# Performance work log

Hardware: AMD Instinct MI355X
Metric: run time of the kernel (lower is better)

Reference implementation:

```python
import jax, jax.numpy as jnp
import numpy as np

B, H, N, D = 64, 12, 196, 768  # ViT-B/16 @ 224: 196 patch tokens + 1 CLS


def setup_inputs() -> dict:
    key = jax.random.key(0)
    k1, k2, k3 = jax.random.split(key, 3)
    student_tokens = jax.random.normal(k1, (B, N, D), dtype=jnp.float32)
    teacher_tokens = jax.random.normal(k2, (B, N, D), dtype=jnp.float32)
    teacher_attn = jax.random.uniform(k3, (B, H, N + 1, N + 1), dtype=jnp.float32)
    return {
        "student_tokens": student_tokens,
        "teacher_tokens": teacher_tokens,
        "teacher_attn": teacher_attn,
    }


def reference(student_tokens, teacher_tokens, teacher_attn):
    s = student_tokens.astype(jnp.float32)
    t = teacher_tokens.astype(jnp.float32)
    # CLS->patch attention, averaged over heads: [B, N]
    w = teacher_attn[:, :, 0, 1:].mean(axis=1)
    w = w / (w.sum(axis=-1, keepdims=True) + 1e-8)
    s = w[..., None] * s
    t = w[..., None] * t
    # center over token dim
    s_c = s - s.mean(axis=1, keepdims=True)
    t_c = t - t.mean(axis=1, keepdims=True)
    tr_s = jnp.sum(s_c * s_c, axis=(1, 2))  # [B]
    tr_t = jnp.sum(t_c * t_c, axis=(1, 2))  # [B]
    # cross-covariance: [B, D, D]
    cross = jnp.einsum("bnd,bne->bde", s_c, t_c)
    # nuclear norm = sum of singular values
    nuclear = jnp.linalg.svd(cross, compute_uv=False).sum(axis=-1)  # [B]
    loss = jnp.maximum(tr_s + tr_t - 2.0 * nuclear, 0.0).mean()
    return loss
```

## Files before the change

### kernel.cpp

```cpp
#include <hip/hip_runtime.h>
#include <hip/hip_bf16.h>
#include <math.h>

#define NTOK 196
#define NDIM 768
#define NB 64
#define NH 12
#define NA 197
#define MAT (NTOK * NTOK)
#define ATTN_HW (NA * NA)
#define POLAR_ITERS 15

#define PADC 208
#define NTILE 13
#define POLAR_LDS_BYTES (2 * NTOK * PADC * 2)

#define GCH 64
#define GPLANE (208 * GCH)
#define GRAM_LDS_BYTES (2 * GPLANE * 2)

#define POW_LD 197
#define POW_F_WORDS (NTOK * POW_LD)
#define POW_LDS_BYTES ((POW_F_WORDS + 2 * NTOK + 256) * 4)

#define PTLD 208
#define TRI_WORDS 19306
#define CHOL2_PT_WORDS (16 * PTLD)
#define CHOL2_TRI_OFF CHOL2_PT_WORDS
#define CHOL2_ROWOFF_OFF (CHOL2_TRI_OFF + TRI_WORDS)
#define CHOL2_PV_OFF 22832
#define CHOL2_LDS_BYTES ((CHOL2_PV_OFF + 32) * 4)

typedef __attribute__((ext_vector_type(8))) short short8;
typedef __attribute__((ext_vector_type(4))) short short4_t;
typedef __attribute__((ext_vector_type(4))) float f32x4;

__device__ inline short8 s8zero() { short8 z = {0,0,0,0,0,0,0,0}; return z; }

__device__ inline short f2bf(float f) {
  union { float f; unsigned u; } v; v.f = f;
  unsigned u = v.u;
  u += 0x7fffu + ((u >> 16) & 1u);
  return (short)(u >> 16);
}
__device__ inline float bf2f(short s) {
  union { unsigned u; float f; } v;
  v.u = ((unsigned)(unsigned short)s) << 16;
  return v.f;
}

__device__ inline int swz_g(int g, int r) {
  if (g < 16) return g ^ (r & 7);
  else if (g < 24) return 16 + ((g - 16) ^ (r & 7));
  else return 24 + ((g - 24) ^ (r & 1));
}

__global__ void k_w(const float* __restrict__ attn, float* __restrict__ wbuf) {
  int b = blockIdx.x;
  int tid = threadIdx.x;
  __shared__ float red[256];
  float w0 = 0.f;
  if (tid < NTOK) {
    size_t base = (size_t)b * NH * ATTN_HW + 1 + tid;
    #pragma unroll
    for (int h = 0; h < NH; ++h) w0 += attn[base + (size_t)h * ATTN_HW];
    w0 *= (1.f / NH);
  }
  red[tid] = (tid < NTOK) ? w0 : 0.f;
  __syncthreads();
  for (int s = 128; s > 0; s >>= 1) { if (tid < s) red[tid] += red[tid + s]; __syncthreads(); }
  float S = red[0];
  if (tid < NTOK) wbuf[b * NTOK + tid] = w0 / (S + 1e-8f);
}

__global__ __launch_bounds__(512, 1) void k_gram_mfma(
    const float* __restrict__ s, const float* __restrict__ t,
    const float* __restrict__ wbuf, float* __restrict__ Gbuf) {
  extern __shared__ short gsm[];
  short* bhp = gsm;
  short* blp = gsm + GPLANE;
  __shared__ float wsh[NTOK];
  int slot = blockIdx.x, b = slot >> 1, src = slot & 1;
  const float* X = (src ? t : s) + (size_t)b * NTOK * NDIM;
  int tid = threadIdx.x;
  int wave = tid >> 6, ln15 = tid & 15, quad = (tid >> 4) & 3;

  if (tid < NTOK) wsh[tid] = wbuf[b * NTOK + tid];
  for (int i = tid; i < 768; i += 512) {
    int p = i / 384, o = i - p * 384;
    ((int*)(gsm + p * GPLANE + 196 * GCH))[o] = 0;
  }
  __syncthreads();

  f32x4 zz = {0.f, 0.f, 0.f, 0.f};
  f32x4 acc[12];
  #pragma unroll
  for (int j = 0; j < 12; ++j) acc[j] = zz;

  for (int c = 0; c < NDIM / GCH; ++c) {
    int kc = c * GCH;
    for (int gi = tid; gi < NTOK * 8; gi += 512) {
      int r = gi >> 3, g = gi & 7;
      const float* sp = X + (size_t)r * NDIM + kc + g * 8;
      float4 f0 = *(const float4*)(sp);
      float4 f1 = *(const float4*)(sp + 4);
      float wv = wsh[r];
      float vs[8] = {f0.x, f0.y, f0.z, f0.w, f1.x, f1.y, f1.z, f1.w};
      short8 hv, lv;
      #pragma unroll
      for (int e = 0; e < 8; ++e) {
        float y = wv * vs[e];
        short hb = f2bf(y);
        hv[e] = hb;
        lv[e] = f2bf(y - bf2f(hb));
      }
      int pg = (g ^ (r & 7)) * 8;
      *(short8*)(bhp + r * GCH + pg) = hv;
      *(short8*)(blp + r * GCH + pg) = lv;
    }
    __syncthreads();
    #pragma unroll
    for (int j = 0; j < 12; ++j) {
      int T = wave + 8 * j;
      if (T < 91) {
        int ti = (int)((sqrtf(8.f * T + 1.f) - 1.f) * 0.5f);
        if ((ti + 1) * (ti + 2) / 2 <= T) ++ti;
        if (ti * (ti + 1) / 2 > T) --ti;
        int tj = T - ti * (ti + 1) / 2;
        int ra = ti * 16 + ln15, rb = tj * 16 + ln15;
        #pragma unroll
        for (int ks = 0; ks < 2; ++ks) {
          int gb0 = ks * 4 + quad;
          int ga = (gb0 ^ (ra & 7)) * 8, gb = (gb0 ^ (rb & 7)) * 8;
          short8 ah = *(const short8*)(bhp + ra * GCH + ga);
          short8 al = *(const short8*)(blp + ra * GCH + ga);
          short8 bhf = *(const short8*)(bhp + rb * GCH + gb);
          short8 blf = *(const short8*)(blp + rb * GCH + gb);
          acc[j] = __builtin_amdgcn_mfma_f32_16x16x32_bf16(ah, bhf, acc[j], 0, 0, 0);
          acc[j] = __builtin_amdgcn_mfma_f32_16x16x32_bf16(ah, blf, acc[j], 0, 0, 0);
          acc[j] = __builtin_amdgcn_mfma_f32_16x16x32_bf16(al, bhf, acc[j], 0, 0, 0);
        }
      }
    }
    __syncthreads();
  }

  float* G = Gbuf + (size_t)slot * MAT;
  #pragma unroll
  for (int j = 0; j < 12; ++j) {
    int T = wave + 8 * j;
    if (T < 91) {
      int ti = (int)((sqrtf(8.f * T + 1.f) - 1.f) * 0.5f);
      if ((ti + 1) * (ti + 2) / 2 <= T) ++ti;
      if (ti * (ti + 1) / 2 > T) --ti;
      int tj = T - ti * (ti + 1) / 2;
      int col = tj * 16 + ln15;
      #pragma unroll
      for (int r = 0; r < 4; ++r) {
        int row = ti * 16 + quad * 4 + r;
        if (row < NTOK && col < NTOK) {
          G[row * NTOK + col] = acc[j][r];
          if (ti != tj) G[col * NTOK + row] = acc[j][r];
        }
      }
    }
  }
}

__global__ void k_center(float* __restrict__ Gbuf, float* __restrict__ trPb) {
  int slot = blockIdx.x;
  float* A = Gbuf + (size_t)slot * MAT;
  __shared__ float r[NTOK];
  __shared__ float red[256];
  __shared__ float gsh, dsh;
  int tid = threadIdx.x;
  float acc = 0.f;
  if (tid < NTOK) {
    for (int m = 0; m < NTOK; ++m) acc += A[m * NTOK + tid];
    r[tid] = acc * (1.f / NTOK);
  }
  red[tid] = (tid < NTOK) ? acc * (1.f / NTOK) : 0.f;
  __syncthreads();
  for (int s = 128; s > 0; s >>= 1) { if (tid < s) red[tid] += red[tid + s]; __syncthreads(); }
  float g = red[0] * (1.f / NTOK);
  float tv = (tid < NTOK) ? (A[tid * NTOK + tid] - 2.f * r[tid] + g) : 0.f;
  __syncthreads();
  red[tid] = tv;
  __syncthreads();
  for (int s = 128; s > 0; s >>= 1) { if (tid < s) red[tid] += red[tid + s]; __syncthreads(); }
  if (tid == 0) {
    float tr = red[0];
    trPb[slot] = tr;
    gsh = g;
    dsh = 1e-4f * fmaxf(tr, 0.f) * (1.f / NTOK);
  }
  __syncthreads();
  float gg = gsh, dd = dsh;
  for (int idx = tid; idx < MAT; idx += 256) {
    int n = idx / NTOK, m = idx - n * NTOK;
    float v = A[idx] - r[n] - r[m] + gg;
    if (n == m) v += dd;
    A[idx] = v;
  }
}

__global__ __launch_bounds__(256, 1) void k_chol_panel(float* __restrict__ Gbuf) {
  extern __shared__ float smf[];
  float* Pt = smf;
  float* tri = smf + CHOL2_TRI_OFF;
  int* rowoff = (int*)(smf + CHOL2_ROWOFF_OFF);
  float* pvb = smf + CHOL2_PV_OFF;
  int slot = blockIdx.x;
  float* A = Gbuf + (size_t)slot * MAT;
  int tid = threadIdx.x;
  if (tid < NTOK) rowoff[tid] = tid * (tid + 1) / 2;
  __syncthreads();
  for (int idx = tid; idx < MAT; idx += 256) {
    int i = idx / NTOK, j = idx - i * NTOK;
    if (j <= i) tri[rowoff[i] + j] = A[idx];
  }
  __syncthreads();

  for (int k0 = 0; k0 < NTOK; k0 += 16) {
    int nb = (NTOK - k0 < 16) ? (NTOK - k0) : 16;
    int t = tid;
    int i = k0 + t;
    bool hasrow = (t < NTOK - k0);
    int ro = hasrow ? rowoff[i] : 0;

    float a[16];
    #pragma unroll
    for (int jj = 0; jj < 16; ++jj) a[jj] = 0.f;
    if (hasrow) {
      #pragma unroll
      for (int jj = 0; jj < 16; ++jj)
        if (jj < nb && k0 + jj <= i) a[jj] = tri[ro + k0 + jj];
    }

    #pragma unroll
    for (int jj = 0; jj < 16; ++jj) {
      bool cv = (jj < nb);
      if (cv && hasrow && t >= jj && t < nb) pvb[((jj & 1) << 4) + t] = a[jj];
      __syncthreads();
      if (cv && hasrow && t >= jj) {
        const float* pv = pvb + ((jj & 1) << 4);
        f32x4 p0 = *(const f32x4*)(pv);
        f32x4 p1 = *(const f32x4*)(pv + 4);
        f32x4 p2 = *(const f32x4*)(pv + 8);
        f32x4 p3 = *(const f32x4*)(pv + 12);
        float pvj = (jj < 4) ? p0[jj & 3] : (jj < 8) ? p1[jj & 3]
                   : (jj < 12) ? p2[jj & 3] : p3[jj & 3];
        float sq = sqrtf(fmaxf(pvj, 1e-20f));
        float pivinv = 1.f / sq;
        float v = a[jj] * pivinv;
        a[jj] = v;
        #pragma unroll
        for (int m = 0; m < 16; ++m) {
          if (m > jj) {
            float pvm = (m < 4) ? p0[m & 3] : (m < 8) ? p1[m & 3]
                       : (m < 12) ? p2[m & 3] : p3[m & 3];
            if (m < nb) a[m] -= v * (pvm * pivinv);
          }
        }
      }
    }

    if (hasrow) {
      #pragma unroll
      for (int jj = 0; jj < 16; ++jj)
        if (jj < nb && k0 + jj <= i) tri[ro + k0 + jj] = a[jj];
      if (t >= nb) {
        #pragma unroll
        for (int jj = 0; jj < 16; ++jj)
          if (jj < nb) Pt[jj * PTLD + i] = a[jj];
      }
    }
    __syncthreads();

    int k1 = k0 + nb;
    int nrem = NTOK - k1;
    if (nrem > 0) {
      int ntile = (nrem + 3) >> 2;
      int Ttot = ntile * (ntile + 1) / 2;
      for (int T = tid; T < Ttot; T += 256) {
        float disc = (2.f * ntile + 1.f) * (2.f * ntile + 1.f) - 8.f * (float)T;
        int tm = (int)((2.f * ntile + 1.f - sqrtf(fmaxf(disc, 0.f))) * 0.5f);
        if (tm > ntile - 1) tm = ntile - 1;
        if (tm < 0) tm = 0;
        #define FCOL(c) ((c) * ntile - (((c) * ((c) - 1)) >> 1))
        while (tm + 1 <= ntile - 1 && FCOL(tm + 1) <= T) ++tm;
        while (tm > 0 && FCOL(tm) > T) --tm;
        int ti = tm + (T - FCOL(tm));
        #undef FCOL
        int i0 = k1 + ti * 4, m0 = k1 + tm * 4;
        f32x4 acc0 = {0.f, 0.f, 0.f, 0.f};
        f32x4 acc1 = acc0, acc2 = acc0, acc3 = acc0;
        #pragma unroll
        for (int jj = 0; jj < 16; ++jj) {
          if (jj < nb) {
            f32x4 li = *(const f32x4*)(Pt + jj * PTLD + i0);
            f32x4 lm = *(const f32x4*)(Pt + jj * PTLD + m0);
            acc0 += lm * li[0];
            acc1 += lm * li[1];
            acc2 += lm * li[2];
            acc3 += lm * li[3];
          }
        }
        #define STORE_ROW(r, av)                                        \
          { int ii = i0 + (r);                                          \
            if (ii < NTOK) {                                            \
              int roi = rowoff[ii];                                     \
              if (m0 + 0 <= ii) tri[roi + m0 + 0] -= (av)[0];           \
              if (m0 + 1 <= ii) tri[roi + m0 + 1] -= (av)[1];           \
              if (m0 + 2 <= ii) tri[roi + m0 + 2] -= (av)[2];           \
              if (m0 + 3 <= ii) tri[roi + m0 + 3] -= (av)[3];           \
            } }
        STORE_ROW(0, acc0)
        STORE_ROW(1, acc1)
        STORE_ROW(2, acc2)
        STORE_ROW(3, acc3)
        #undef STORE_ROW
      }
    }
    __syncthreads();
  }

  for (int idx = tid; idx < MAT; idx += 256) {
    int i = idx / NTOK, j = idx - i * NTOK;
    A[idx] = (j <= i) ? tri[rowoff[i] + j] : 0.f;
  }
}

__global__ void k_chol_global(float* __restrict__ Gbuf) {
  int slot = blockIdx.x;
  float* A = Gbuf + (size_t)slot * MAT;
  __shared__ float col[NTOK];
  __shared__ float piv;
  int tid = threadIdx.x;
  for (int k = 0; k < NTOK; ++k) {
    if (tid == 0) { float p = sqrtf(fmaxf(A[k * NTOK + k], 1e-20f)); A[k * NTOK + k] = p; piv = p; }
    __syncthreads();
    float inv = 1.f / piv;
    for (int i = k + 1 + tid; i < NTOK; i += 256) {
      float v = A[i * NTOK + k] * inv;
      A[i * NTOK + k] = v;
      col[i] = v;
    }
    for (int j = k + 1 + tid; j < NTOK; j += 256) A[k * NTOK + j] = 0.f;
    __syncthreads();
    int nrem = NTOK - 1 - k;
    int total = nrem * (nrem + 1) / 2;
    for (int tt = tid; tt < total; tt += 256) {
      int a = (int)((sqrtf(8.f * tt + 1.f) - 1.f) * 0.5f);
      while ((a + 1) * (a + 2) / 2 <= tt) ++a;
      while (a * (a + 1) / 2 > tt) --a;
      int bb = tt - a * (a + 1) / 2;
      int i = k + 1 + a, j = k + 1 + bb;
      A[i * NTOK + j] -= col[i] * col[j];
    }
    __syncthreads();
  }
}

__global__ void k_F(const float* __restrict__ Gbuf, float* __restrict__ Fbuf) {
  int b = blockIdx.y;
  const float* Lp = Gbuf + (size_t)(2 * b) * MAT;
  const float* Lq = Gbuf + (size_t)(2 * b + 1) * MAT;
  int ti = blockIdx.x / 7, tj = blockIdx.x % 7;
  int ri = ti * 32, cj = tj * 32;
  __shared__ float As[32][33], Bs[32][33];
  int tid = threadIdx.x, ty = tid >> 4, tx = tid & 15;
  float a00 = 0, a01 = 0, a10 = 0, a11 = 0;
  for (int k0 = 0; k0 < NTOK; k0 += 32) {
    for (int l = tid; l < 1024; l += 256) {
      int kk = l >> 5, ii = l & 31;
      int krow = k0 + kk;
      As[kk][ii] = (krow < NTOK && ri + ii < NTOK) ? Lp[(size_t)krow * NTOK + ri + ii] : 0.f;
      Bs[kk][ii] = (krow < NTOK && cj + ii < NTOK) ? Lq[(size_t)krow * NTOK + cj + ii] : 0.f;
    }
    __syncthreads();
    #pragma unroll
    for (int kk = 0; kk < 32; ++kk) {
      float p0 = As[kk][ty], p1 = As[kk][ty + 16];
      float q0 = Bs[kk][tx], q1 = Bs[kk][tx + 16];
      a00 += p0 * q0; a01 += p0 * q1; a10 += p1 * q0; a11 += p1 * q1;
    }
    __syncthreads();
  }
  float* F = Fbuf + (size_t)b * MAT;
  int i0 = ri + ty, i1 = ri + ty + 16, j0 = cj + tx, j1 = cj + tx + 16;
  if (i0 < NTOK && j0 < NTOK) F[i0 * NTOK + j0] = a00;
  if (i0 < NTOK && j1 < NTOK) F[i0 * NTOK + j1] = a01;
  if (i1 < NTOK && j0 < NTOK) F[i1 * NTOK + j0] = a10;
  if (i1 < NTOK && j1 < NTOK) F[i1 * NTOK + j1] = a11;
}

__global__ __launch_bounds__(256, 1) void k_pow_lds(const float* __restrict__ Fbuf,
                                                    float* __restrict__ nrmb) {
  extern __shared__ float psm[];
  float* Fsh = psm;
  float* v = psm + POW_F_WORDS;
  float* u = v + NTOK;
  float* red = u + NTOK;
  int b = blockIdx.x;
  const float* F = Fbuf + (size_t)b * MAT;
  int tid = threadIdx.x;
  for (int idx = tid; idx < MAT; idx += 256) {
    int i = idx / NTOK, j = idx - i * NTOK;
    Fsh[i * POW_LD + j] = F[idx];
  }
  if (tid < NTOK) v[tid] = 1.f;
  __syncthreads();
  float lastsum = 1.f;
  for (int it = 0; it < 6; ++it) {
    if (tid < NTOK) {
      float a = 0.f;
      for (int j = 0; j < NTOK; ++j) a += Fsh[tid * POW_LD + j] * v[j];
      u[tid] = a;
    }
    __syncthreads();
    float a2 = 0.f;
    if (tid < NTOK) { for (int i = 0; i < NTOK; ++i) a2 += Fsh[i * POW_LD + tid] * u[i]; }
    red[tid] = (tid < NTOK) ? a2 * a2 : 0.f;
    __syncthreads();
    for (int s2 = 128; s2 > 0; s2 >>= 1) { if (tid < s2) red[tid] += red[tid + s2]; __syncthreads(); }
    float sum = red[0];
    lastsum = sum;
    float invn = rsqrtf(sum + 1e-30f);
    __syncthreads();
    if (tid < NTOK) v[tid] = a2 * invn;
    __syncthreads();
  }
  if (tid == 0) {
    float sig = sqrtf(sqrtf(lastsum));
    nrmb[b] = 1.f / (1.1f * sig + 1e-30f);
  }
}

__global__ void k_pow(const float* __restrict__ Fbuf, float* __restrict__ nrmb) {
  int b = blockIdx.x;
  const float* F = Fbuf + (size_t)b * MAT;
  __shared__ float v[NTOK], u[NTOK];
  __shared__ float red[256];
  int tid = threadIdx.x;
  if (tid < NTOK) v[tid] = 1.f;
  __syncthreads();
  float lastsum = 1.f;
  for (int it = 0; it < 6; ++it) {
    float a = 0.f;
    if (tid < NTOK) { for (int j = 0; j < NTOK; ++j) a += F[tid * NTOK + j] * v[j]; }
    __syncthreads();
    if (tid < NTOK) u[tid] = a;
    __syncthreads();
    float a2 = 0.f;
    if (tid < NTOK) { for (int i = 0; i < NTOK; ++i) a2 += F[i * NTOK + tid] * u[i]; }
    red[tid] = (tid < NTOK) ? a2 * a2 : 0.f;
    __syncthreads();
    for (int s = 128; s > 0; s >>= 1) { if (tid < s) red[tid] += red[tid + s]; __syncthreads(); }
    float sum = red[0];
    lastsum = sum;
    float invn = rsqrtf(sum + 1e-30f);
    __syncthreads();
    if (tid < NTOK) v[tid] = a2 * invn;
    __syncthreads();
  }
  if (tid == 0) {
    float sig = sqrtf(sqrtf(lastsum));
    nrmb[b] = 1.f / (1.1f * sig + 1e-30f);
  }
}

__global__ void k_scale(const float* __restrict__ Fbuf, const float* __restrict__ nrmb,
                        float* __restrict__ X) {
  int b = blockIdx.y;
  int idx = blockIdx.x * 256 + threadIdx.x;
  if (idx < MAT) X[(size_t)b * MAT + idx] = Fbuf[(size_t)b * MAT + idx] * nrmb[b];
}

__global__ __launch_bounds__(512, 1) void k_polar_fused(
    const float* __restrict__ Fbuf, const float* __restrict__ nrmb,
    float* __restrict__ Xout) {
  extern __shared__ short sm[];
  short* bufA = sm;
  short* bufB = sm + NTOK * PADC;
  int b = blockIdx.x;
  const float* F = Fbuf + (size_t)b * MAT;
  float* XO = Xout + (size_t)b * MAT;
  int tid = threadIdx.x;
  int wave = tid >> 6, ln15 = tid & 15, quad = (tid >> 4) & 3;
  int rt0 = wave, rt1 = wave + 8;
  bool has2 = (rt1 < NTILE);

  for (int i = tid; i < (2 * NTOK * PADC) / 2; i += 512) ((int*)sm)[i] = 0;
  __syncthreads();
  float invc = nrmb[b];
  for (int idx = tid; idx < MAT; idx += 512) {
    int i = idx / NTOK, j = idx - i * NTOK;
    bufA[i * PADC + swz_g(j >> 3, i) * 8 + (j & 7)] = f2bf(F[idx] * invc);
  }
  __syncthreads();

  int arow0 = rt0 * 16 + ln15;
  int arow1 = rt1 * 16 + ln15;
  bool av1 = has2 && (arow1 < NTOK);
  int m0a = rt0 * 16 + quad * 4;
  int m1a = rt1 * 16 + quad * 4;
  int gq0 = 2 * rt0 + (quad >> 1);
  int gq1 = 2 * rt1 + (quad >> 1);
  int wsub = (quad & 1) * 4;
  int ga0 = arow0 >> 3, go0 = arow0 & 7;
  int ga1 = arow1 >> 3, go1 = arow1 & 7;

  for (int it = 0; it < POLAR_ITERS; ++it) {
    {
      short8 a0[7], a1[7];
      #pragma unroll
      for (int ks = 0; ks < 7; ++ks) {
        int kk = ks * 32 + quad * 8;
        int g = ks * 4 + quad;
        a0[ks] = (kk < PADC) ? *(const short8*)(bufA + arow0 * PADC + swz_g(g, arow0) * 8)
                             : s8zero();
        a1[ks] = (av1 && kk < PADC)
                     ? *(const short8*)(bufA + arow1 * PADC + swz_g(g, arow1) * 8)
                     : s8zero();
      }
      for (int ct = 0; ct < NTILE; ++ct) {
        int brow = ct * 16 + ln15;
        bool bv = brow < NTOK;
        f32x4 acc0 = {0.f, 0.f, 0.f, 0.f};
        f32x4 acc1 = {0.f, 0.f, 0.f, 0.f};
        #pragma unroll
        for (int ks = 0; ks < 7; ++ks) {
          int kk = ks * 32 + quad * 8;
          int g = ks * 4 + quad;
          short8 bfr = (bv && kk < PADC)
                           ? *(const short8*)(bufA + brow * PADC + swz_g(g, brow) * 8)
                           : s8zero();
          acc0 = __builtin_amdgcn_mfma_f32_16x16x32_bf16(a0[ks], bfr, acc0, 0, 0, 0);
          if (has2)
            acc1 = __builtin_amdgcn_mfma_f32_16x16x32_bf16(a1[ks], bfr, acc1, 0, 0, 0);
        }
        if (bv) {
          short4_t w0;
          #pragma unroll
          for (int r = 0; r < 4; ++r) {
            float h = -0.5f * acc0[r] + ((m0a + r == brow) ? 1.5f : 0.f);
            w0[r] = f2bf(h);
          }
          *(short4_t*)(bufB + brow * PADC + swz_g(gq0, brow) * 8 + wsub) = w0;
          if (has2) {
            short4_t w1;
            #pragma unroll
            for (int r = 0; r < 4; ++r) {
              float h = -0.5f * acc1[r] + ((m1a + r == brow) ? 1.5f : 0.f);
              w1[r] = f2bf(h);
            }
            *(short4_t*)(bufB + brow * PADC + swz_g(gq1, brow) * 8 + wsub) = w1;
          }
        }
      }
    }
    __syncthreads();
    {
      short8 g0[7], g1[7];
      #pragma unroll
      for (int ks = 0; ks < 7; ++ks) {
        int kk = ks * 32 + quad * 8;
        short8 v0 = s8zero(), v1 = s8zero();
        if (kk < PADC) {
          #pragma unroll
          for (int j = 0; j < 8; ++j) {
            int rr = kk + j;
            v0[j] = bufA[rr * PADC + swz_g(ga0, rr) * 8 + go0];
            if (has2) v1[j] = bufA[rr * PADC + swz_g(ga1, rr) * 8 + go1];
          }
        }
        g0[ks] = v0; g1[ks] = v1;
      }
      __syncthreads();
      for (int ct = 0; ct < NTILE; ++ct) {
        int n = ct * 16 + ln15;
        bool nv = n < NTOK;
        f32x4 acc0 = {0.f, 0.f, 0.f, 0.f};
        f32x4 acc1 = {0.f, 0.f, 0.f, 0.f};
        #pragma unroll
        for (int ks = 0; ks < 7; ++ks) {
          int kk = ks * 32 + quad * 8;
          int g = ks * 4 + quad;
          short8 bfr = (nv && kk < PADC)
                           ? *(const short8*)(bufB + n * PADC + swz_g(g, n) * 8)
                           : s8zero();
          acc0 = __builtin_amdgcn_mfma_f32_16x16x32_bf16(g0[ks], bfr, acc0, 0, 0, 0);
          if (has2)
            acc1 = __builtin_amdgcn_mfma_f32_16x16x32_bf16(g1[ks], bfr, acc1, 0, 0, 0);
        }
        if (nv) {
          short4_t w0;
          #pragma unroll
          for (int r = 0; r < 4; ++r) w0[r] = f2bf(acc0[r]);
          *(short4_t*)(bufA + n * PADC + swz_g(gq0, n) * 8 + wsub) = w0;
          if (has2) {
            short4_t w1;
            #pragma unroll
            for (int r = 0; r < 4; ++r) w1[r] = f2bf(acc1[r]);
            *(short4_t*)(bufA + n * PADC + swz_g(gq1, n) * 8 + wsub) = w1;
          }
        }
      }
    }
    __syncthreads();
  }

  for (int idx = tid; idx < MAT; idx += 512) {
    int i = idx / NTOK, j = idx - i * NTOK;
    XO[idx] = bf2f(bufA[i * PADC + swz_g(j >> 3, i) * 8 + (j & 7)]);
  }
}

__global__ void k_xtx(const float* __restrict__ Xb, float* __restrict__ Gp) {
  int b = blockIdx.y;
  const float* X = Xb + (size_t)b * MAT;
  int x = blockIdx.x, ti = 0;
  while (x >= ti + 1) { x -= ti + 1; ++ti; }
  int tj = x;
  int ri = ti * 32, cj = tj * 32;
  __shared__ float As[32][33], Bs[32][33];
  int tid = threadIdx.x, ty = tid >> 4, tx = tid & 15;
  float a00 = 0, a01 = 0, a10 = 0, a11 = 0;
  for (int k0 = 0; k0 < NTOK; k0 += 32) {
    for (int l = tid; l < 1024; l += 256) {
      int kk = l >> 5, ii = l & 31;
      int krow = k0 + kk;
      As[kk][ii] = (krow < NTOK && ri + ii < NTOK) ? X[(size_t)krow * NTOK + ri + ii] : 0.f;
      Bs[kk][ii] = (krow < NTOK && cj + ii < NTOK) ? X[(size_t)krow * NTOK + cj + ii] : 0.f;
    }
    __syncthreads();
    #pragma unroll
    for (int kk = 0; kk < 32; ++kk) {
      float p0 = As[kk][ty], p1 = As[kk][ty + 16];
      float q0 = Bs[kk][tx], q1 = Bs[kk][tx + 16];
      a00 += p0 * q0; a01 += p0 * q1; a10 += p1 * q0; a11 += p1 * q1;
    }
    __syncthreads();
  }
  float* G = Gp + (size_t)b * MAT;
  int i0 = ri + ty, i1 = ri + ty + 16, j0 = cj + tx, j1 = cj + tx + 16;
  if (i0 < NTOK && j0 < NTOK) { G[i0 * NTOK + j0] = a00; G[j0 * NTOK + i0] = a00; }
  if (i0 < NTOK && j1 < NTOK) { G[i0 * NTOK + j1] = a01; G[j1 * NTOK + i0] = a01; }
  if (i1 < NTOK && j0 < NTOK) { G[i1 * NTOK + j0] = a10; G[j0 * NTOK + i1] = a10; }
  if (i1 < NTOK && j1 < NTOK) { G[i1 * NTOK + j1] = a11; G[j1 * NTOK + i1] = a11; }
}

__global__ void k_nsup(const float* __restrict__ Xb, const float* __restrict__ Gp,
                       float* __restrict__ Xn) {
  int b = blockIdx.y;
  const float* X = Xb + (size_t)b * MAT;
  const float* G = Gp + (size_t)b * MAT;
  int ti = blockIdx.x / 7, tj = blockIdx.x % 7;
  int ri = ti * 32, cj = tj * 32;
  __shared__ float As[32][33], Bs[32][33];
  int tid = threadIdx.x, ty = tid >> 4, tx = tid & 15;
  float a00 = 0, a01 = 0, a10 = 0, a11 = 0;
  for (int k0 = 0; k0 < NTOK; k0 += 32) {
    for (int l = tid; l < 1024; l += 256) {
      int rr = l >> 5, cc = l & 31;
      As[rr][cc] = (ri + rr < NTOK && k0 + cc < NTOK) ? X[(size_t)(ri + rr) * NTOK + k0 + cc] : 0.f;
      Bs[rr][cc] = (k0 + rr < NTOK && cj + cc < NTOK) ? G[(size_t)(k0 + rr) * NTOK + cj + cc] : 0.f;
    }
    __syncthreads();
    #pragma unroll
    for (int kk = 0; kk < 32; ++kk) {
      float p0 = As[ty][kk], p1 = As[ty + 16][kk];
      float q0 = Bs[kk][tx], q1 = Bs[kk][tx + 16];
      a00 += p0 * q0; a01 += p0 * q1; a10 += p1 * q0; a11 += p1 * q1;
    }
    __syncthreads();
  }
  float* O = Xn + (size_t)b * MAT;
  int i0 = ri + ty, i1 = ri + ty + 16, j0 = cj + tx, j1 = cj + tx + 16;
  if (i0 < NTOK && j0 < NTOK) O[i0 * NTOK + j0] = 1.5f * X[i0 * NTOK + j0] - 0.5f * a00;
  if (i0 < NTOK && j1 < NTOK) O[i0 * NTOK + j1] = 1.5f * X[i0 * NTOK + j1] - 0.5f * a01;
  if (i1 < NTOK && j0 < NTOK) O[i1 * NTOK + j0] = 1.5f * X[i1 * NTOK + j0] - 0.5f * a10;
  if (i1 < NTOK && j1 < NTOK) O[i1 * NTOK + j1] = 1.5f * X[i1 * NTOK + j1] - 0.5f * a11;
}

__global__ void k_nuc(const float* __restrict__ U, const float* __restrict__ Fbuf,
                      float* __restrict__ nucb) {
  int b = blockIdx.x;
  int tid = threadIdx.x;
  const float* Ub = U + (size_t)b * MAT;
  const float* Fb = Fbuf + (size_t)b * MAT;
  float acc = 0.f;
  for (int idx = tid; idx < MAT; idx += 256) acc += Ub[idx] * Fb[idx];
  __shared__ float red[256];
  red[tid] = acc;
  __syncthreads();
  for (int s = 128; s > 0; s >>= 1) { if (tid < s) red[tid] += red[tid + s]; __syncthreads(); }
  if (tid == 0) nucb[b] = red[0];
}

__global__ void k_final(const float* __restrict__ trPb, const float* __restrict__ nucb,
                        float* __restrict__ out) {
  int tid = threadIdx.x;
  float v = fmaxf(trPb[2 * tid] + trPb[2 * tid + 1] - 2.f * nucb[tid], 0.f);
  #pragma unroll
  for (int off = 32; off; off >>= 1) v += __shfl_down(v, off);
  if (tid == 0) out[0] = v * (1.f / 64.f);
}

extern "C" void kernel_launch(void* const* d_in, const int* in_sizes, int n_in,
                              void* d_out, int out_size, void* d_ws, size_t ws_size,
                              hipStream_t stream) {
  (void)in_sizes; (void)n_in; (void)out_size; (void)ws_size;
  const float* s = (const float*)d_in[0];
  const float* t = (const float*)d_in[1];
  const float* attn = (const float*)d_in[2];
  float* out = (float*)d_out;

  float* W = (float*)d_ws;
  float* Gbuf = W;
  float* Fbuf = Gbuf + (size_t)128 * MAT;
  float* Xbuf = Fbuf + (size_t)64 * MAT;
  float* Xnew = Xbuf + (size_t)64 * MAT;
  float* Gpol = Xnew + (size_t)64 * MAT;
  float* wbuf = Gpol + (size_t)64 * MAT;
  float* trPb = wbuf + (size_t)NB * NTOK;
  float* nucb = trPb + 128;
  float* nrmb = nucb + 64;

  k_w<<<NB, 256, 0, stream>>>(attn, wbuf);
  k_gram_mfma<<<128, 512, GRAM_LDS_BYTES, stream>>>(s, t, wbuf, Gbuf);
  k_center<<<128, 256, 0, stream>>>(Gbuf, trPb);

  hipError_t chol_ok = hipFuncSetAttribute(
      reinterpret_cast<const void*>(k_chol_panel),
      hipFuncAttributeMaxDynamicSharedMemorySize, CHOL2_LDS_BYTES);
  if (chol_ok == hipSuccess) {
    k_chol_panel<<<128, 256, CHOL2_LDS_BYTES, stream>>>(Gbuf);
  } else {
    k_chol_global<<<128, 256, 0, stream>>>(Gbuf);
  }

  k_F<<<dim3(49, 64), 256, 0, stream>>>(Gbuf, Fbuf);

  hipError_t pow_ok = hipFuncSetAttribute(
      reinterpret_cast<const void*>(k_pow_lds),
      hipFuncAttributeMaxDynamicSharedMemorySize, POW_LDS_BYTES);
  if (pow_ok == hipSuccess) {
    k_pow_lds<<<64, 256, POW_LDS_BYTES, stream>>>(Fbuf, nrmb);
  } else {
    k_pow<<<64, 256, 0, stream>>>(Fbuf, nrmb);
  }

  hipError_t fused_ok = hipFuncSetAttribute(
      reinterpret_cast<const void*>(k_polar_fused),
      hipFuncAttributeMaxDynamicSharedMemorySize, POLAR_LDS_BYTES);

  const float* finalX;
  if (fused_ok == hipSuccess) {
    k_polar_fused<<<NB, 512, POLAR_LDS_BYTES, stream>>>(Fbuf, nrmb, Xbuf);
    k_xtx<<<dim3(28, 64), 256, 0, stream>>>(Xbuf, Gpol);
    k_nsup<<<dim3(49, 64), 256, 0, stream>>>(Xbuf, Gpol, Xnew);
    k_xtx<<<dim3(28, 64), 256, 0, stream>>>(Xnew, Gpol);
    k_nsup<<<dim3(49, 64), 256, 0, stream>>>(Xnew, Gpol, Xbuf);
    finalX = Xbuf;
  } else {
    k_scale<<<dim3(151, 64), 256, 0, stream>>>(Fbuf, nrmb, Xbuf);
    float* Xc = Xbuf;
    float* Xn = Xnew;
    for (int it = 0; it < POLAR_ITERS; ++it) {
      k_xtx<<<dim3(28, 64), 256, 0, stream>>>(Xc, Gpol);
      k_nsup<<<dim3(49, 64), 256, 0, stream>>>(Xc, Gpol, Xn);
      float* tmp = Xc; Xc = Xn; Xn = tmp;
    }
    finalX = Xc;
  }

  k_nuc<<<64, 256, 0, stream>>>(finalX, Fbuf, nucb);
  k_final<<<1, 64, 0, stream>>>(trPb, nucb, out);
}
```

Baseline: 1.015 ms.

## Rework fused polar kernel to 4 waves with 4 row tiles each and B-fragment reuse

The fused Newton-Schulz polar kernel drops from 512 to 256 threads, so each wave now owns up to four 16-row tiles instead of two. Each loaded B fragment therefore feeds four MFMAs, and when the column tile equals one of the wave's own row tiles the already-loaded A registers are reused in place of an LDS read. The XOR swizzle on the LDS layout is removed for plain row-major indexing, and the global load/store and LDS zeroing are vectorised to float4/int4. The trade-offs are much higher register pressure per lane, fewer waves per block to hide latency, and possible LDS bank conflicts now that the swizzle is gone, especially on the strided column gathers.

Result: slower. 1.049 ms (+3.3%).

```diff
diff --git a/kernel.cpp b/kernel.cpp
--- a/kernel.cpp
+++ b/kernel.cpp
@@ -47,12 +47,6 @@
   union { unsigned u; float f; } v;
   v.u = ((unsigned)(unsigned short)s) << 16;
   return v.f;
-}
-
-__device__ inline int swz_g(int g, int r) {
-  if (g < 16) return g ^ (r & 7);
-  else if (g < 24) return 16 + ((g - 16) ^ (r & 7));
-  else return 24 + ((g - 24) ^ (r & 1));
 }
 
 __global__ void k_w(const float* __restrict__ attn, float* __restrict__ wbuf) {
@@ -477,7 +471,7 @@
   if (idx < MAT) X[(size_t)b * MAT + idx] = Fbuf[(size_t)b * MAT + idx] * nrmb[b];
 }
 
-__global__ __launch_bounds__(512, 1) void k_polar_fused(
+__global__ __launch_bounds__(256, 1) void k_polar_fused(
     const float* __restrict__ Fbuf, const float* __restrict__ nrmb,
     float* __restrict__ Xout) {
   extern __shared__ short sm[];
@@ -488,122 +482,141 @@
   float* XO = Xout + (size_t)b * MAT;
   int tid = threadIdx.x;
   int wave = tid >> 6, ln15 = tid & 15, quad = (tid >> 4) & 3;
-  int rt0 = wave, rt1 = wave + 8;
-  bool has2 = (rt1 < NTILE);
-
-  for (int i = tid; i < (2 * NTOK * PADC) / 2; i += 512) ((int*)sm)[i] = 0;
+
+  int tA[4]; bool tv[4]; int arow[4]; bool av[4]; int mcol[4];
+  #pragma unroll
+  for (int s = 0; s < 4; ++s) {
+    tA[s] = wave + 4 * s;
+    tv[s] = (tA[s] < NTILE);
+    arow[s] = tA[s] * 16 + ln15;
+    av[s] = tv[s] && (arow[s] < NTOK);
+    mcol[s] = tA[s] * 16 + quad * 4;
+  }
+
+  for (int q = tid; q < (2 * NTOK * PADC) / 8; q += 256) {
+    int4 z = {0, 0, 0, 0};
+    ((int4*)sm)[q] = z;
+  }
   __syncthreads();
   float invc = nrmb[b];
-  for (int idx = tid; idx < MAT; idx += 512) {
+  for (int q = tid; q < MAT / 4; q += 256) {
+    int idx = q * 4;
     int i = idx / NTOK, j = idx - i * NTOK;
-    bufA[i * PADC + swz_g(j >> 3, i) * 8 + (j & 7)] = f2bf(F[idx] * invc);
-  }
-  __syncthreads();
-
-  int arow0 = rt0 * 16 + ln15;
-  int arow1 = rt1 * 16 + ln15;
-  bool av1 = has2 && (arow1 < NTOK);
-  int m0a = rt0 * 16 + quad * 4;
-  int m1a = rt1 * 16 + quad * 4;
-  int gq0 = 2 * rt0 + (quad >> 1);
-  int gq1 = 2 * rt1 + (quad >> 1);
-  int wsub = (quad & 1) * 4;
-  int ga0 = arow0 >> 3, go0 = arow0 & 7;
-  int ga1 = arow1 >> 3, go1 = arow1 & 7;
+    float4 f = ((const float4*)F)[q];
+    short4_t w;
+    w[0] = f2bf(f.x * invc); w[1] = f2bf(f.y * invc);
+    w[2] = f2bf(f.z * invc); w[3] = f2bf(f.w * invc);
+    *(short4_t*)(bufA + i * PADC + j) = w;
+  }
+  __syncthreads();
 
   for (int it = 0; it < POLAR_ITERS; ++it) {
     {
-      short8 a0[7], a1[7];
+      short8 a[4][7];
       #pragma unroll
-      for (int ks = 0; ks < 7; ++ks) {
-        int kk = ks * 32 + quad * 8;
-        int g = ks * 4 + quad;
-        a0[ks] = (kk < PADC) ? *(const short8*)(bufA + arow0 * PADC + swz_g(g, arow0) * 8)
-                             : s8zero();
-        a1[ks] = (av1 && kk < PADC)
-                     ? *(const short8*)(bufA + arow1 * PADC + swz_g(g, arow1) * 8)
-                     : s8zero();
+      for (int s = 0; s < 4; ++s) {
+        #pragma unroll
+        for (int ks = 0; ks < 7; ++ks) {
+          int kk = ks * 32 + quad * 8;
+          a[s][ks] = (av[s] && kk < PADC)
+                         ? *(const short8*)(bufA + arow[s] * PADC + kk) : s8zero();
+        }
       }
       for (int ct = 0; ct < NTILE; ++ct) {
         int brow = ct * 16 + ln15;
         bool bv = brow < NTOK;
-        f32x4 acc0 = {0.f, 0.f, 0.f, 0.f};
-        f32x4 acc1 = {0.f, 0.f, 0.f, 0.f};
+        short8 bfr[7];
+        if (ct == tA[0]) {
+          #pragma unroll
+          for (int ks = 0; ks < 7; ++ks) bfr[ks] = a[0][ks];
+        } else if (ct == tA[1]) {
+          #pragma unroll
+          for (int ks = 0; ks < 7; ++ks) bfr[ks] = a[1][ks];
+        } else if (ct == tA[2]) {
+          #pragma unroll
+          for (int ks = 0; ks < 7; ++ks) bfr[ks] = a[2][ks];
+        } else if (ct == tA[3]) {
+          #pragma unroll
+          for (int ks = 0; ks < 7; ++ks) bfr[ks] = a[3][ks];
+        } else {
+          #pragma unroll
+          for (int ks = 0; ks < 7; ++ks) {
+            int kk = ks * 32 + quad * 8;
+            bfr[ks] = (bv && kk < PADC)
+                          ? *(const short8*)(bufA + brow * PADC + kk) : s8zero();
+          }
+        }
+        f32x4 acc[4];
+        #pragma unroll
+        for (int s = 0; s < 4; ++s) { f32x4 z = {0.f, 0.f, 0.f, 0.f}; acc[s] = z; }
+        #pragma unroll
+        for (int ks = 0; ks < 7; ++ks) {
+          #pragma unroll
+          for (int s = 0; s < 4; ++s)
+            acc[s] = __builtin_amdgcn_mfma_f32_16x16x32_bf16(a[s][ks], bfr[ks], acc[s], 0, 0, 0);
+        }
+        if (bv) {
+          #pragma unroll
+          for (int s = 0; s < 4; ++s) {
+            if (tv[s]) {
+              short4_t w;
+              #pragma unroll
+              for (int r = 0; r < 4; ++r) {
+                float h = -0.5f * acc[s][r] + ((mcol[s] + r == brow) ? 1.5f : 0.f);
+                w[r] = f2bf(h);
+              }
+              *(short4_t*)(bufB + brow * PADC + mcol[s]) = w;
+            }
+          }
+        }
+      }
+    }
+    __syncthreads();
+    {
+      short8 g[4][7];
+      #pragma unroll
+      for (int s = 0; s < 4; ++s) {
         #pragma unroll
         for (int ks = 0; ks < 7; ++ks) {
           int kk = ks * 32 + quad * 8;
-          int g = ks * 4 + quad;
-          short8 bfr = (bv && kk < PADC)
-                           ? *(const short8*)(bufA + brow * PADC + swz_g(g, brow) * 8)
-                           : s8zero();
-          acc0 = __builtin_amdgcn_mfma_f32_16x16x32_bf16(a0[ks], bfr, acc0, 0, 0, 0);
-          if (has2)
-            acc1 = __builtin_amdgcn_mfma_f32_16x16x32_bf16(a1[ks], bfr, acc1, 0, 0, 0);
-        }
-        if (bv) {
-          short4_t w0;
-          #pragma unroll
-          for (int r = 0; r < 4; ++r) {
-            float h = -0.5f * acc0[r] + ((m0a + r == brow) ? 1.5f : 0.f);
-            w0[r] = f2bf(h);
+          short8 v = s8zero();
+          if (tv[s] && kk < PADC) {
+            #pragma unroll
+            for (int j = 0; j < 8; ++j)
+              v[j] = bufA[(kk + j) * PADC + arow[s]];
           }
-          *(short4_t*)(bufB + brow * PADC + swz_g(gq0, brow) * 8 + wsub) = w0;
-          if (has2) {
-            short4_t w1;
-            #pragma unroll
-            for (int r = 0; r < 4; ++r) {
-              float h = -0.5f * acc1[r] + ((m1a + r == brow) ? 1.5f : 0.f);
-              w1[r] = f2bf(h);
-            }
-            *(short4_t*)(bufB + brow * PADC + swz_g(gq1, brow) * 8 + wsub) = w1;
-          }
-        }
-      }
-    }
-    __syncthreads();
-    {
-      short8 g0[7], g1[7];
-      #pragma unroll
-      for (int ks = 0; ks < 7; ++ks) {
-        int kk = ks * 32 + quad * 8;
-        short8 v0 = s8zero(), v1 = s8zero();
-        if (kk < PADC) {
-          #pragma unroll
-          for (int j = 0; j < 8; ++j) {
-            int rr = kk + j;
-            v0[j] = bufA[rr * PADC + swz_g(ga0, rr) * 8 + go0];
-            if (has2) v1[j] = bufA[rr * PADC + swz_g(ga1, rr) * 8 + go1];
-          }
-        }
-        g0[ks] = v0; g1[ks] = v1;
+          g[s][ks] = v;
+        }
       }
       __syncthreads();
       for (int ct = 0; ct < NTILE; ++ct) {
         int n = ct * 16 + ln15;
         bool nv = n < NTOK;
-        f32x4 acc0 = {0.f, 0.f, 0.f, 0.f};
-        f32x4 acc1 = {0.f, 0.f, 0.f, 0.f};
+        short8 bfr[7];
         #pragma unroll
         for (int ks = 0; ks < 7; ++ks) {
           int kk = ks * 32 + quad * 8;
-          int g = ks * 4 + quad;
-          short8 bfr = (nv && kk < PADC)
-                           ? *(const short8*)(bufB + n * PADC + swz_g(g, n) * 8)
-                           : s8zero();
-          acc0 = __builtin_amdgcn_mfma_f32_16x16x32_bf16(g0[ks], bfr, acc0, 0, 0, 0);
-          if (has2)
-            acc1 = __builtin_amdgcn_mfma_f32_16x16x32_bf16(g1[ks], bfr, acc1, 0, 0, 0);
+          bfr[ks] = (nv && kk < PADC)
+                        ? *(const short8*)(bufB + n * PADC + kk) : s8zero();
+        }
+        f32x4 acc[4];
+        #pragma unroll
+        for (int s = 0; s < 4; ++s) { f32x4 z = {0.f, 0.f, 0.f, 0.f}; acc[s] = z; }
+        #pragma unroll
+        for (int ks = 0; ks < 7; ++ks) {
+          #pragma unroll
+          for (int s = 0; s < 4; ++s)
+            acc[s] = __builtin_amdgcn_mfma_f32_16x16x32_bf16(g[s][ks], bfr[ks], acc[s], 0, 0, 0);
         }
         if (nv) {
-          short4_t w0;
-          #pragma unroll
-          for (int r = 0; r < 4; ++r) w0[r] = f2bf(acc0[r]);
-          *(short4_t*)(bufA + n * PADC + swz_g(gq0, n) * 8 + wsub) = w0;
-          if (has2) {
-            short4_t w1;
-            #pragma unroll
-            for (int r = 0; r < 4; ++r) w1[r] = f2bf(acc1[r]);
-            *(short4_t*)(bufA + n * PADC + swz_g(gq1, n) * 8 + wsub) = w1;
+          #pragma unroll
+          for (int s = 0; s < 4; ++s) {
+            if (tv[s]) {
+              short4_t w;
+              #pragma unroll
+              for (int r = 0; r < 4; ++r) w[r] = f2bf(acc[s][r]);
+              *(short4_t*)(bufA + n * PADC + mcol[s]) = w;
+            }
           }
         }
       }
@@ -611,9 +624,13 @@
     __syncthreads();
   }
 
-  for (int idx = tid; idx < MAT; idx += 512) {
+  for (int q = tid; q < MAT / 4; q += 256) {
+    int idx = q * 4;
     int i = idx / NTOK, j = idx - i * NTOK;
-    XO[idx] = bf2f(bufA[i * PADC + swz_g(j >> 3, i) * 8 + (j & 7)]);
+    short4_t w = *(const short4_t*)(bufA + i * PADC + j);
+    float4 f;
+    f.x = bf2f(w[0]); f.y = bf2f(w[1]); f.z = bf2f(w[2]); f.w = bf2f(w[3]);
+    ((float4*)XO)[q] = f;
   }
 }
 
@@ -758,7 +775,7 @@
 
   const float* finalX;
   if (fused_ok == hipSuccess) {
-    k_polar_fused<<<NB, 512, POLAR_LDS_BYTES, stream>>>(Fbuf, nrmb, Xbuf);
+    k_polar_fused<<<NB, 256, POLAR_LDS_BYTES, stream>>>(Fbuf, nrmb, Xbuf);
     k_xtx<<<dim3(28, 64), 256, 0, stream>>>(Xbuf, Gpol);
     k_nsup<<<dim3(49, 64), 256, 0, stream>>>(Xbuf, Gpol, Xnew);
     k_xtx<<<dim3(28, 64), 256, 0, stream>>>(Xnew, Gpol);
```
